# Optimization experiments

Hardware: AMD Instinct MI355X
Metric: run time of the kernel (lower is better)

The kernel has to match this reference:

```python
import jax, jax.numpy as jnp
import numpy as np

K = 3        # neighborhood kernel per spatial dim
DIL = 1      # dilation per spatial dim
NH = 8       # num heads
C = 64       # embed dims
EPS = 1e-5   # InstanceNorm eps


def _interp_axis(x, axis, out_len):
    # 1D linear interpolation with align_corners=True semantics
    in_len = x.shape[axis]
    pos = jnp.arange(out_len, dtype=jnp.float32) * ((in_len - 1) / (out_len - 1))
    i0 = jnp.clip(jnp.floor(pos).astype(jnp.int32), 0, in_len - 2)
    w = pos - i0.astype(jnp.float32)
    shape = [1] * x.ndim
    shape[axis] = out_len
    w = w.reshape(shape)
    return jnp.take(x, i0, axis=axis) * (1.0 - w) + jnp.take(x, i0 + 1, axis=axis) * w


def _upsample2_trilinear(x):
    # separable trilinear upsample x2 over the three spatial axes (2,3,4)
    for ax in (2, 3, 4):
        x = _interp_axis(x, ax, 2 * x.shape[ax])
    return x


def _instance_norm(t):
    # InstanceNorm3d, affine=False: normalize per (B,C) over spatial dims
    m = jnp.mean(t, axis=(2, 3, 4), keepdims=True)
    v = jnp.var(t, axis=(2, 3, 4), keepdims=True)
    return (t - m) * jax.lax.rsqrt(v + EPS)


def _nbr_idx(L, k, d):
    # NATTEN-style clamped neighborhood: window shifts to stay in-bounds at edges
    i = np.arange(L)
    start = np.clip(i - d * (k // 2), 0, L - d * (k - 1) - 1)
    idx = start[:, None] + np.arange(k)[None, :] * d          # (L,k) absolute nbr index
    rel = (idx - i[:, None]) // d + (k - 1)                   # (L,k) rel-pos-bias index in [0,2k-2]
    return jnp.asarray(idx), jnp.asarray(rel)


def _nca3d(qs, kv, Wq, bq, Wk, bk, Wv, bv, Wo, bo, rpb):
    # qs, kv: (B,H,W,Z,C) channels-last; q from skip, k/v from upsampled x
    B, H, W, Z, Cc = qs.shape
    dh = Cc // NH
    scale = dh ** -0.5
    q = (qs @ Wq + bq).reshape(B, H, W, Z, NH, dh) * scale
    k = (kv @ Wk + bk).reshape(B, H, W, Z, NH, dh)
    v = (kv @ Wv + bv).reshape(B, H, W, Z, NH, dh)

    ih, rh = _nbr_idx(H, K, DIL)
    iw, rw = _nbr_idx(W, K, DIL)
    iz, rz = _nbr_idx(Z, K, DIL)

    def gather_nbrs(t):
        t = jnp.take(t, ih, axis=1)   # (B,H,k,W,Z,nh,dh)
        t = jnp.take(t, iw, axis=3)   # (B,H,k,W,k,Z,nh,dh)
        t = jnp.take(t, iz, axis=5)   # (B,H,k,W,k,Z,k,nh,dh)
        t = jnp.transpose(t, (0, 1, 3, 5, 7, 2, 4, 6, 8))
        return t.reshape(B, H, W, Z, NH, K * K * K, dh)

    kg = gather_nbrs(k)
    vg = gather_nbrs(v)

    logits = jnp.einsum('bxyzhd,bxyzhmd->bxyzhm', q, kg)  # (B,H,W,Z,nh,27)

    # relative position bias: rpb (nh, 2k-1, 2k-1, 2k-1) gathered per query position
    bias = rpb[:, rh]                    # (nh,H,k,2k-1,2k-1)
    bias = jnp.take(bias, rw, axis=3)    # (nh,H,k,W,k,2k-1)
    bias = jnp.take(bias, rz, axis=5)    # (nh,H,k,W,k,Z,k)
    bias = jnp.transpose(bias, (1, 3, 5, 0, 2, 4, 6)).reshape(H, W, Z, NH, K * K * K)

    attn = jax.nn.softmax(logits + bias, axis=-1)
    o = jnp.einsum('bxyzhm,bxyzhmd->bxyzhd', attn, vg).reshape(B, H, W, Z, Cc)
    o = o @ Wo + bo
    return jnp.transpose(o, (0, 4, 1, 2, 3))  # back to (B,C,H,W,Z)


def setup_inputs() -> dict:
    key = jax.random.key(0)
    ks = jax.random.split(key, 8)
    s = 1.0 / np.sqrt(C)
    inp = {
        'x': jax.random.normal(ks[0], (1, C, 32, 32, 8), dtype=jnp.float32),
        'skip': jax.random.normal(ks[1], (1, C, 64, 64, 16), dtype=jnp.float32),
        'Wq': jax.random.normal(ks[2], (C, C), dtype=jnp.float32) * s,
        'bq': jnp.zeros((C,), dtype=jnp.float32),
        'Wk': jax.random.normal(ks[3], (C, C), dtype=jnp.float32) * s,
        'bk': jnp.zeros((C,), dtype=jnp.float32),
        'Wv': jax.random.normal(ks[4], (C, C), dtype=jnp.float32) * s,
        'bv': jnp.zeros((C,), dtype=jnp.float32),
        'Wo': jax.random.normal(ks[5], (C, C), dtype=jnp.float32) * s,
        'bo': jnp.zeros((C,), dtype=jnp.float32),
        'rpb': jax.random.normal(ks[6], (NH, 2 * K - 1, 2 * K - 1, 2 * K - 1), dtype=jnp.float32) * 0.02,
    }
    return inp


def reference(x, skip, Wq, bq, Wk, bk, Wv, bv, Wo, bo, rpb):
    xu = _instance_norm(_upsample2_trilinear(x))   # (B,C,2H,2W,2Z) == skip shape
    sk = _instance_norm(skip)
    qs = jnp.transpose(sk, (0, 2, 3, 4, 1))        # queries from skip
    kv = jnp.transpose(xu, (0, 2, 3, 4, 1))        # keys/values from upsampled x
    return _nca3d(qs, kv, Wq, bq, Wk, bk, Wv, bv, Wo, bo, rpb)
```

## Files before the change

### kernel.cpp

```cpp
#include <hip/hip_runtime.h>
#include <hip/hip_bf16.h>

typedef __hip_bfloat16 bf16;
typedef __attribute__((ext_vector_type(8))) short short8;

static constexpr int NPOS = 65536;

__device__ __forceinline__ float bs2f(short s) {
  union { float f; unsigned u; } cv;
  cv.u = ((unsigned)(unsigned short)s) << 16;
  return cv.f;
}
__device__ __forceinline__ short f2bs(float f) {
  bf16 b = __float2bfloat16(f);
  short r;
  __builtin_memcpy(&r, &b, 2);
  return r;
}

__global__ __launch_bounds__(256) void k_partial(const float* __restrict__ x,
                                                 const float* __restrict__ skip,
                                                 bf16* __restrict__ xu,
                                                 float* __restrict__ partials) {
  __shared__ float s1[256];
  __shared__ float s2[256];
  int b = blockIdx.x, tid = threadIdx.x;
  float sum = 0.f, sq = 0.f;
  if (b < 1024) {
    int c = b >> 4;
    int h = (b & 15) * 4 + (tid >> 6);
    int w = tid & 63;
    float fh = (float)h * (31.0f / 63.0f);
    int ih = (int)fh; if (ih > 30) ih = 30;
    float wh = fh - (float)ih;
    float fw = (float)w * (31.0f / 63.0f);
    int iw = (int)fw; if (iw > 30) iw = 30;
    float ww = fw - (float)iw;
    const float* base = x + c * 8192 + ih * 256 + iw * 8;
    float4 A0 = *(const float4*)(base);
    float4 A1 = *(const float4*)(base + 4);
    float4 B0 = *(const float4*)(base + 8);
    float4 B1 = *(const float4*)(base + 12);
    float4 C0 = *(const float4*)(base + 256);
    float4 C1 = *(const float4*)(base + 260);
    float4 D0 = *(const float4*)(base + 264);
    float4 D1 = *(const float4*)(base + 268);
    float ra[8] = {A0.x, A0.y, A0.z, A0.w, A1.x, A1.y, A1.z, A1.w};
    float rb[8] = {B0.x, B0.y, B0.z, B0.w, B1.x, B1.y, B1.z, B1.w};
    float rc[8] = {C0.x, C0.y, C0.z, C0.w, C1.x, C1.y, C1.z, C1.w};
    float rd[8] = {D0.x, D0.y, D0.z, D0.w, D1.x, D1.y, D1.z, D1.w};
    short8 o0, o1;
#pragma unroll
    for (int z = 0; z < 16; z++) {
      float fz = (float)z * (7.0f / 15.0f);
      int iz = (int)fz; if (iz > 6) iz = 6;
      float wz = fz - (float)iz;
      float va = ra[iz] * (1.f - wz) + ra[iz + 1] * wz;
      float vb = rb[iz] * (1.f - wz) + rb[iz + 1] * wz;
      float vc = rc[iz] * (1.f - wz) + rc[iz + 1] * wz;
      float vd = rd[iz] * (1.f - wz) + rd[iz + 1] * wz;
      float v0 = va * (1.f - ww) + vb * ww;
      float v1 = vc * (1.f - ww) + vd * ww;
      float v = v0 * (1.f - wh) + v1 * wh;
      sum += v; sq += v * v;
      if (z < 8) o0[z] = f2bs(v); else o1[z - 8] = f2bs(v);
    }
    bf16* xo = xu + (size_t)c * NPOS + h * 1024 + w * 16;
    *(short8*)xo = o0;
    *(short8*)(xo + 8) = o1;
  } else {
    int bb = b - 1024;
    const float4* p =
        (const float4*)(skip + (size_t)(bb >> 4) * NPOS + (bb & 15) * 4096);
    for (int i = tid; i < 1024; i += 256) {
      float4 v = p[i];
      sum += v.x + v.y + v.z + v.w;
      sq += v.x * v.x + v.y * v.y + v.z * v.z + v.w * v.w;
    }
  }
  s1[tid] = sum; s2[tid] = sq;
  __syncthreads();
  for (int s = 128; s > 0; s >>= 1) {
    if (tid < s) { s1[tid] += s1[tid + s]; s2[tid] += s2[tid + s]; }
    __syncthreads();
  }
  if (tid == 0) { partials[2 * b] = s1[0]; partials[2 * b + 1] = s2[0]; }
}

__global__ __launch_bounds__(128) void k_finalize(const float* __restrict__ partials,
                                                  float* __restrict__ stats) {
  int t = threadIdx.x;
  int base = (t < 64) ? t * 16 : 1024 + (t - 64) * 16;
  float sum = 0.f, sq = 0.f;
#pragma unroll
  for (int j = 0; j < 16; j++) {
    sum += partials[2 * (base + j)];
    sq  += partials[2 * (base + j) + 1];
  }
  float m = sum * (1.0f / NPOS);
  float var = sq * (1.0f / NPOS) - m * m;
  int off = (t < 64) ? 0 : 128;
  int c = t & 63;
  stats[off + c] = m;
  stats[off + 64 + c] = rsqrtf(var + 1e-5f);
}

__global__ __launch_bounds__(256) void k_proj_kvq(
    const bf16* __restrict__ xu, const float* __restrict__ skip,
    const float* __restrict__ stats,
    const float* __restrict__ Wk, const float* __restrict__ bk,
    const float* __restrict__ Wv, const float* __restrict__ bv,
    const float* __restrict__ Wq, const float* __restrict__ bq,
    bf16* __restrict__ kbuf, bf16* __restrict__ vbuf, bf16* __restrict__ qbuf) {
  __shared__ float xt[4096];
  int tid = threadIdx.x;
  int p0 = blockIdx.x * 64;
  for (int ii = tid; ii < 512; ii += 256) {
    int c = ii >> 3, t0 = (ii & 7) * 8;
    short8 v8 = *(const short8*)(xu + (size_t)c * NPOS + p0 + t0);
    float m = stats[c], r = stats[64 + c];
#pragma unroll
    for (int u = 0; u < 8; u++) xt[c * 64 + t0 + u] = (bs2f(v8[u]) - m) * r;
  }
  __syncthreads();
  int t = tid & 63;
  int j0 = __builtin_amdgcn_readfirstlane((tid >> 6) * 16);
  size_t p = (size_t)(p0 + t);
  float a[16];
  short8 s0, s1v;

#pragma unroll
  for (int u = 0; u < 16; u++) a[u] = bk[j0 + u];
  for (int c = 0; c < 64; c++) {
    float xv = xt[c * 64 + t];
    const float* wr = Wk + c * 64 + j0;
#pragma unroll
    for (int u = 0; u < 16; u++) a[u] += xv * wr[u];
  }
#pragma unroll
  for (int u = 0; u < 8; u++) { s0[u] = f2bs(a[u]); s1v[u] = f2bs(a[8 + u]); }
  *(short8*)(kbuf + p * 64 + j0) = s0;
  *(short8*)(kbuf + p * 64 + j0 + 8) = s1v;

#pragma unroll
  for (int u = 0; u < 16; u++) a[u] = bv[j0 + u];
  for (int c = 0; c < 64; c++) {
    float xv = xt[c * 64 + t];
    const float* wr = Wv + c * 64 + j0;
#pragma unroll
    for (int u = 0; u < 16; u++) a[u] += xv * wr[u];
  }
#pragma unroll
  for (int u = 0; u < 8; u++) { s0[u] = f2bs(a[u]); s1v[u] = f2bs(a[8 + u]); }
  *(short8*)(vbuf + p * 64 + j0) = s0;
  *(short8*)(vbuf + p * 64 + j0 + 8) = s1v;

  __syncthreads();
  for (int ii = tid; ii < 1024; ii += 256) {
    int c = ii >> 4, t0 = (ii & 15) * 4;
    float4 v = *(const float4*)(skip + (size_t)c * NPOS + p0 + t0);
    float m = stats[128 + c], r = stats[192 + c];
    xt[c * 64 + t0]     = (v.x - m) * r;
    xt[c * 64 + t0 + 1] = (v.y - m) * r;
    xt[c * 64 + t0 + 2] = (v.z - m) * r;
    xt[c * 64 + t0 + 3] = (v.w - m) * r;
  }
  __syncthreads();

  const float scale = 0.35355339059327373f;
#pragma unroll
  for (int u = 0; u < 16; u++) a[u] = bq[j0 + u];
  for (int c = 0; c < 64; c++) {
    float xv = xt[c * 64 + t];
    const float* wr = Wq + c * 64 + j0;
#pragma unroll
    for (int u = 0; u < 16; u++) a[u] += xv * wr[u];
  }
#pragma unroll
  for (int u = 0; u < 8; u++) {
    s0[u] = f2bs(a[u] * scale); s1v[u] = f2bs(a[8 + u] * scale);
  }
  *(short8*)(qbuf + p * 64 + j0) = s0;
  *(short8*)(qbuf + p * 64 + j0 + 8) = s1v;
}

__global__ __launch_bounds__(512, 2) void k_attn(
    const bf16* __restrict__ qbuf, const bf16* __restrict__ kbuf,
    const bf16* __restrict__ vbuf,
    const float* __restrict__ Wo, const float* __restrict__ bo,
    const float* __restrict__ rpb, float* __restrict__ out) {
  __shared__ float rp[1000];
  __shared__ float oT[64 * 65];
  int tid = threadIdx.x;
  int b = blockIdx.x;
  int sb = ((b & 7) << 7) + (b >> 3);
  int p0 = sb * 64;
  for (int i = tid; i < 1000; i += 512) rp[i] = rpb[i];
  __syncthreads();

  int head = tid & 7, pp = tid >> 3;
  int p = p0 + pp;
  int h = p >> 10, w = (p >> 4) & 63, z = p & 15;

  short8 q8 = *(const short8*)(qbuf + (size_t)p * 64 + head * 8);
  float q[8];
#pragma unroll
  for (int d = 0; d < 8; d++) q[d] = bs2f(q8[d]);

  int sh = h - 1; if (sh < 0) sh = 0; if (sh > 61) sh = 61;
  int sw = w - 1; if (sw < 0) sw = 0; if (sw > 61) sw = 61;
  int sz = z - 1; if (sz < 0) sz = 0; if (sz > 13) sz = 13;

  const bf16* kb = kbuf + (size_t)(sh * 1024 + sw * 16 + sz) * 64 + head * 8;
  const bf16* vb = vbuf + (size_t)(sh * 1024 + sw * 16 + sz) * 64 + head * 8;
  int rbase = ((sh - h + 2) * 5 + (sw - w + 2)) * 5 + (sz - z + 2) + head * 125;

  float s[27];
#pragma unroll
  for (int j = 0; j < 27; j++) {
    int kh = j / 9, kw = (j % 9) / 3, kz = j % 3;
    int coff = (kh * 1024 + kw * 16 + kz) * 64;
    short8 k8 = *(const short8*)(kb + coff);
    float sv = q[0] * bs2f(k8[0]) + q[1] * bs2f(k8[1]) +
               q[2] * bs2f(k8[2]) + q[3] * bs2f(k8[3]) +
               q[4] * bs2f(k8[4]) + q[5] * bs2f(k8[5]) +
               q[6] * bs2f(k8[6]) + q[7] * bs2f(k8[7]);
    s[j] = sv + rp[rbase + (kh * 5 + kw) * 5 + kz];
  }
  float M = s[26];
#pragma unroll
  for (int j = 0; j < 13; j++) M = fmaxf(M, fmaxf(s[2 * j], s[2 * j + 1]));

  float lrun = 0.f;
  float oa[8];
#pragma unroll
  for (int d = 0; d < 8; d++) oa[d] = 0.f;
#pragma unroll
  for (int j = 0; j < 27; j++) {
    int kh = j / 9, kw = (j % 9) / 3, kz = j % 3;
    int coff = (kh * 1024 + kw * 16 + kz) * 64;
    short8 v8 = *(const short8*)(vb + coff);
    float pw = __expf(s[j] - M);
    lrun += pw;
#pragma unroll
    for (int d = 0; d < 8; d++) oa[d] += pw * bs2f(v8[d]);
  }
  float inv = 1.0f / lrun;
#pragma unroll
  for (int d = 0; d < 8; d++) oT[pp * 65 + head * 8 + d] = oa[d] * inv;
  __syncthreads();

  int wid = __builtin_amdgcn_readfirstlane(tid >> 6);
  int l = tid & 63;
  float acc[8];
#pragma unroll
  for (int u = 0; u < 8; u++) acc[u] = bo[wid * 8 + u];
  for (int j = 0; j < 64; j++) {
    float ov = oT[l * 65 + j];
    const float* wr = Wo + j * 64 + wid * 8;
#pragma unroll
    for (int u = 0; u < 8; u++) acc[u] += ov * wr[u];
  }
#pragma unroll
  for (int u = 0; u < 8; u++)
    out[(size_t)(wid * 8 + u) * NPOS + p0 + l] = acc[u];
}

extern "C" void kernel_launch(void* const* d_in, const int* in_sizes, int n_in,
                              void* d_out, int out_size, void* d_ws, size_t ws_size,
                              hipStream_t stream) {
  const float* x    = (const float*)d_in[0];
  const float* skip = (const float*)d_in[1];
  const float* Wq   = (const float*)d_in[2];
  const float* bq   = (const float*)d_in[3];
  const float* Wk   = (const float*)d_in[4];
  const float* bk   = (const float*)d_in[5];
  const float* Wv   = (const float*)d_in[6];
  const float* bv   = (const float*)d_in[7];
  const float* Wo   = (const float*)d_in[8];
  const float* bo   = (const float*)d_in[9];
  const float* rpb  = (const float*)d_in[10];

  bf16* xu        = (bf16*)d_ws;
  bf16* kbuf      = (bf16*)((char*)d_ws + ((size_t)8 << 20));
  bf16* vbuf      = (bf16*)((char*)d_ws + ((size_t)16 << 20));
  bf16* qbuf      = (bf16*)((char*)d_ws + ((size_t)24 << 20));
  float* stats    = (float*)((char*)d_ws + ((size_t)32 << 20));
  float* partials = stats + 256;
  float* out = (float*)d_out;

  hipLaunchKernelGGL(k_partial, dim3(2048), dim3(256), 0, stream, x, skip, xu,
                     partials);
  hipLaunchKernelGGL(k_finalize, dim3(1), dim3(128), 0, stream, partials, stats);
  hipLaunchKernelGGL(k_proj_kvq, dim3(1024), dim3(256), 0, stream, xu, skip,
                     stats, Wk, bk, Wv, bv, Wq, bq, kbuf, vbuf, qbuf);
  hipLaunchKernelGGL(k_attn, dim3(1024), dim3(512), 0, stream, qbuf, kbuf, vbuf,
                     Wo, bo, rpb, out);
}
```

Measured before the change: 159.7 us.

## Use bf16 MFMA for QKV projections and fold stats finalize into projection kernel

Replaces the scalar FP32 FMA loops of the K/V/Q projections with bf16 MFMA 16x16x32 instructions. Activations and weights are staged in padded LDS tiles, and outputs are written to LDS and then stored with coalesced stores. The separate single-block finalize kernel is removed: each projection block recomputes the per-channel mean and rstd from the partial sums, which saves a launch and a serial tiny kernel. In exchange, inputs and weights are rounded to bf16 before the matmul, which lowers precision, and every block redundantly reads the partials and converts the weights.

```diff
diff --git a/kernel.cpp b/kernel.cpp
--- a/kernel.cpp
+++ b/kernel.cpp
@@ -3,6 +3,7 @@
 
 typedef __hip_bfloat16 bf16;
 typedef __attribute__((ext_vector_type(8))) short short8;
+typedef __attribute__((ext_vector_type(4))) float f32x4;
 
 static constexpr int NPOS = 65536;
 
@@ -87,101 +88,161 @@
   if (tid == 0) { partials[2 * b] = s1[0]; partials[2 * b + 1] = s2[0]; }
 }
 
-__global__ __launch_bounds__(128) void k_finalize(const float* __restrict__ partials,
-                                                  float* __restrict__ stats) {
-  int t = threadIdx.x;
-  int base = (t < 64) ? t * 16 : 1024 + (t - 64) * 16;
-  float sum = 0.f, sq = 0.f;
-#pragma unroll
-  for (int j = 0; j < 16; j++) {
-    sum += partials[2 * (base + j)];
-    sq  += partials[2 * (base + j) + 1];
-  }
-  float m = sum * (1.0f / NPOS);
-  float var = sq * (1.0f / NPOS) - m * m;
-  int off = (t < 64) ? 0 : 128;
-  int c = t & 63;
-  stats[off + c] = m;
-  stats[off + 64 + c] = rsqrtf(var + 1e-5f);
-}
-
-__global__ __launch_bounds__(256) void k_proj_kvq(
+__global__ __launch_bounds__(256) void k_proj_mfma(
     const bf16* __restrict__ xu, const float* __restrict__ skip,
-    const float* __restrict__ stats,
+    const float* __restrict__ partials,
     const float* __restrict__ Wk, const float* __restrict__ bk,
     const float* __restrict__ Wv, const float* __restrict__ bv,
     const float* __restrict__ Wq, const float* __restrict__ bq,
     bf16* __restrict__ kbuf, bf16* __restrict__ vbuf, bf16* __restrict__ qbuf) {
-  __shared__ float xt[4096];
+  __shared__ float stl[256];
+  __shared__ short xa[64 * 72];
+  __shared__ short wb[64 * 72];
+  __shared__ short ob[64 * 72];
   int tid = threadIdx.x;
   int p0 = blockIdx.x * 64;
+
+  if (tid < 128) {
+    int isk = tid >> 6, c = tid & 63;
+    int base = isk ? (1024 + c * 16) : (c * 16);
+    float sum = 0.f, sq = 0.f;
+#pragma unroll
+    for (int j = 0; j < 16; j++) {
+      sum += partials[2 * (base + j)];
+      sq  += partials[2 * (base + j) + 1];
+    }
+    float m = sum * (1.0f / NPOS);
+    float var = sq * (1.0f / NPOS) - m * m;
+    stl[isk * 128 + c] = m;
+    stl[isk * 128 + 64 + c] = rsqrtf(var + 1e-5f);
+  }
+  __syncthreads();
+
   for (int ii = tid; ii < 512; ii += 256) {
     int c = ii >> 3, t0 = (ii & 7) * 8;
     short8 v8 = *(const short8*)(xu + (size_t)c * NPOS + p0 + t0);
-    float m = stats[c], r = stats[64 + c];
-#pragma unroll
-    for (int u = 0; u < 8; u++) xt[c * 64 + t0 + u] = (bs2f(v8[u]) - m) * r;
-  }
-  __syncthreads();
-  int t = tid & 63;
-  int j0 = __builtin_amdgcn_readfirstlane((tid >> 6) * 16);
-  size_t p = (size_t)(p0 + t);
-  float a[16];
-  short8 s0, s1v;
-
-#pragma unroll
-  for (int u = 0; u < 16; u++) a[u] = bk[j0 + u];
-  for (int c = 0; c < 64; c++) {
-    float xv = xt[c * 64 + t];
-    const float* wr = Wk + c * 64 + j0;
-#pragma unroll
-    for (int u = 0; u < 16; u++) a[u] += xv * wr[u];
-  }
-#pragma unroll
-  for (int u = 0; u < 8; u++) { s0[u] = f2bs(a[u]); s1v[u] = f2bs(a[8 + u]); }
-  *(short8*)(kbuf + p * 64 + j0) = s0;
-  *(short8*)(kbuf + p * 64 + j0 + 8) = s1v;
-
-#pragma unroll
-  for (int u = 0; u < 16; u++) a[u] = bv[j0 + u];
-  for (int c = 0; c < 64; c++) {
-    float xv = xt[c * 64 + t];
-    const float* wr = Wv + c * 64 + j0;
-#pragma unroll
-    for (int u = 0; u < 16; u++) a[u] += xv * wr[u];
-  }
-#pragma unroll
-  for (int u = 0; u < 8; u++) { s0[u] = f2bs(a[u]); s1v[u] = f2bs(a[8 + u]); }
-  *(short8*)(vbuf + p * 64 + j0) = s0;
-  *(short8*)(vbuf + p * 64 + j0 + 8) = s1v;
-
-  __syncthreads();
+    float m = stl[c], r = stl[64 + c];
+#pragma unroll
+    for (int u = 0; u < 8; u++) xa[(t0 + u) * 72 + c] = f2bs((bs2f(v8[u]) - m) * r);
+  }
+  {
+    int c = tid >> 2, j0 = (tid & 3) * 16;
+    const float4* wr = (const float4*)(Wk + c * 64 + j0);
+    float4 w0 = wr[0], w1 = wr[1], w2 = wr[2], w3 = wr[3];
+    float wv[16] = {w0.x,w0.y,w0.z,w0.w, w1.x,w1.y,w1.z,w1.w,
+                    w2.x,w2.y,w2.z,w2.w, w3.x,w3.y,w3.z,w3.w};
+#pragma unroll
+    for (int u = 0; u < 16; u++) wb[(j0 + u) * 72 + c] = f2bs(wv[u]);
+  }
+  __syncthreads();
+
+  int wv_ = tid >> 6, lane = tid & 63, quad = lane >> 4, l15 = lane & 15;
+  const short* arow = &xa[(wv_ * 16 + l15) * 72 + quad * 8];
+  int orow0 = (wv_ * 16 + quad * 4);
+
+  {
+    short8 a0 = *(const short8*)(arow);
+    short8 a1 = *(const short8*)(arow + 32);
+#pragma unroll
+    for (int nt = 0; nt < 4; nt++) {
+      const short* brow = &wb[(nt * 16 + l15) * 72 + quad * 8];
+      short8 b0 = *(const short8*)(brow);
+      short8 b1 = *(const short8*)(brow + 32);
+      f32x4 acc = {0.f, 0.f, 0.f, 0.f};
+      acc = __builtin_amdgcn_mfma_f32_16x16x32_bf16(a0, b0, acc, 0, 0, 0);
+      acc = __builtin_amdgcn_mfma_f32_16x16x32_bf16(a1, b1, acc, 0, 0, 0);
+      float bval = bk[nt * 16 + l15];
+#pragma unroll
+      for (int r = 0; r < 4; r++)
+        ob[(orow0 + r) * 72 + nt * 16 + l15] = f2bs(acc[r] + bval);
+    }
+  }
+  __syncthreads();
+  {
+    int row = tid >> 2, col0 = (tid & 3) * 16;
+    short8 o0 = *(const short8*)(&ob[row * 72 + col0]);
+    short8 o1 = *(const short8*)(&ob[row * 72 + col0 + 8]);
+    *(short8*)(kbuf + (size_t)(p0 + row) * 64 + col0) = o0;
+    *(short8*)(kbuf + (size_t)(p0 + row) * 64 + col0 + 8) = o1;
+    int c = tid >> 2, j0 = (tid & 3) * 16;
+    const float4* wr = (const float4*)(Wv + c * 64 + j0);
+    float4 w0 = wr[0], w1 = wr[1], w2 = wr[2], w3 = wr[3];
+    float wvv[16] = {w0.x,w0.y,w0.z,w0.w, w1.x,w1.y,w1.z,w1.w,
+                     w2.x,w2.y,w2.z,w2.w, w3.x,w3.y,w3.z,w3.w};
+#pragma unroll
+    for (int u = 0; u < 16; u++) wb[(j0 + u) * 72 + c] = f2bs(wvv[u]);
+  }
+  __syncthreads();
+  {
+    short8 a0 = *(const short8*)(arow);
+    short8 a1 = *(const short8*)(arow + 32);
+#pragma unroll
+    for (int nt = 0; nt < 4; nt++) {
+      const short* brow = &wb[(nt * 16 + l15) * 72 + quad * 8];
+      short8 b0 = *(const short8*)(brow);
+      short8 b1 = *(const short8*)(brow + 32);
+      f32x4 acc = {0.f, 0.f, 0.f, 0.f};
+      acc = __builtin_amdgcn_mfma_f32_16x16x32_bf16(a0, b0, acc, 0, 0, 0);
+      acc = __builtin_amdgcn_mfma_f32_16x16x32_bf16(a1, b1, acc, 0, 0, 0);
+      float bval = bv[nt * 16 + l15];
+#pragma unroll
+      for (int r = 0; r < 4; r++)
+        ob[(orow0 + r) * 72 + nt * 16 + l15] = f2bs(acc[r] + bval);
+    }
+  }
+  __syncthreads();
+  {
+    int row = tid >> 2, col0 = (tid & 3) * 16;
+    short8 o0 = *(const short8*)(&ob[row * 72 + col0]);
+    short8 o1 = *(const short8*)(&ob[row * 72 + col0 + 8]);
+    *(short8*)(vbuf + (size_t)(p0 + row) * 64 + col0) = o0;
+    *(short8*)(vbuf + (size_t)(p0 + row) * 64 + col0 + 8) = o1;
+  }
   for (int ii = tid; ii < 1024; ii += 256) {
     int c = ii >> 4, t0 = (ii & 15) * 4;
     float4 v = *(const float4*)(skip + (size_t)c * NPOS + p0 + t0);
-    float m = stats[128 + c], r = stats[192 + c];
-    xt[c * 64 + t0]     = (v.x - m) * r;
-    xt[c * 64 + t0 + 1] = (v.y - m) * r;
-    xt[c * 64 + t0 + 2] = (v.z - m) * r;
-    xt[c * 64 + t0 + 3] = (v.w - m) * r;
-  }
-  __syncthreads();
-
-  const float scale = 0.35355339059327373f;
-#pragma unroll
-  for (int u = 0; u < 16; u++) a[u] = bq[j0 + u];
-  for (int c = 0; c < 64; c++) {
-    float xv = xt[c * 64 + t];
-    const float* wr = Wq + c * 64 + j0;
-#pragma unroll
-    for (int u = 0; u < 16; u++) a[u] += xv * wr[u];
-  }
-#pragma unroll
-  for (int u = 0; u < 8; u++) {
-    s0[u] = f2bs(a[u] * scale); s1v[u] = f2bs(a[8 + u] * scale);
-  }
-  *(short8*)(qbuf + p * 64 + j0) = s0;
-  *(short8*)(qbuf + p * 64 + j0 + 8) = s1v;
+    float m = stl[128 + c], r = stl[192 + c];
+    xa[(t0 + 0) * 72 + c] = f2bs((v.x - m) * r);
+    xa[(t0 + 1) * 72 + c] = f2bs((v.y - m) * r);
+    xa[(t0 + 2) * 72 + c] = f2bs((v.z - m) * r);
+    xa[(t0 + 3) * 72 + c] = f2bs((v.w - m) * r);
+  }
+  {
+    int c = tid >> 2, j0 = (tid & 3) * 16;
+    const float4* wr = (const float4*)(Wq + c * 64 + j0);
+    float4 w0 = wr[0], w1 = wr[1], w2 = wr[2], w3 = wr[3];
+    float wq_[16] = {w0.x,w0.y,w0.z,w0.w, w1.x,w1.y,w1.z,w1.w,
+                     w2.x,w2.y,w2.z,w2.w, w3.x,w3.y,w3.z,w3.w};
+#pragma unroll
+    for (int u = 0; u < 16; u++) wb[(j0 + u) * 72 + c] = f2bs(wq_[u]);
+  }
+  __syncthreads();
+  {
+    const float scale = 0.35355339059327373f;
+    short8 a0 = *(const short8*)(arow);
+    short8 a1 = *(const short8*)(arow + 32);
+#pragma unroll
+    for (int nt = 0; nt < 4; nt++) {
+      const short* brow = &wb[(nt * 16 + l15) * 72 + quad * 8];
+      short8 b0 = *(const short8*)(brow);
+      short8 b1 = *(const short8*)(brow + 32);
+      f32x4 acc = {0.f, 0.f, 0.f, 0.f};
+      acc = __builtin_amdgcn_mfma_f32_16x16x32_bf16(a0, b0, acc, 0, 0, 0);
+      acc = __builtin_amdgcn_mfma_f32_16x16x32_bf16(a1, b1, acc, 0, 0, 0);
+      float bval = bq[nt * 16 + l15];
+#pragma unroll
+      for (int r = 0; r < 4; r++)
+        ob[(orow0 + r) * 72 + nt * 16 + l15] = f2bs((acc[r] + bval) * scale);
+    }
+  }
+  __syncthreads();
+  {
+    int row = tid >> 2, col0 = (tid & 3) * 16;
+    short8 o0 = *(const short8*)(&ob[row * 72 + col0]);
+    short8 o1 = *(const short8*)(&ob[row * 72 + col0 + 8]);
+    *(short8*)(qbuf + (size_t)(p0 + row) * 64 + col0) = o0;
+    *(short8*)(qbuf + (size_t)(p0 + row) * 64 + col0 + 8) = o1;
+  }
 }
 
 __global__ __launch_bounds__(512, 2) void k_attn(
@@ -285,15 +346,13 @@
   bf16* kbuf      = (bf16*)((char*)d_ws + ((size_t)8 << 20));
   bf16* vbuf      = (bf16*)((char*)d_ws + ((size_t)16 << 20));
   bf16* qbuf      = (bf16*)((char*)d_ws + ((size_t)24 << 20));
-  float* stats    = (float*)((char*)d_ws + ((size_t)32 << 20));
-  float* partials = stats + 256;
+  float* partials = (float*)((char*)d_ws + ((size_t)32 << 20));
   float* out = (float*)d_out;
 
   hipLaunchKernelGGL(k_partial, dim3(2048), dim3(256), 0, stream, x, skip, xu,
                      partials);
-  hipLaunchKernelGGL(k_finalize, dim3(1), dim3(128), 0, stream, partials, stats);
-  hipLaunchKernelGGL(k_proj_kvq, dim3(1024), dim3(256), 0, stream, xu, skip,
-                     stats, Wk, bk, Wv, bv, Wq, bq, kbuf, vbuf, qbuf);
+  hipLaunchKernelGGL(k_proj_mfma, dim3(1024), dim3(256), 0, stream, xu, skip,
+                     partials, Wk, bk, Wv, bv, Wq, bq, kbuf, vbuf, qbuf);
   hipLaunchKernelGGL(k_attn, dim3(1024), dim3(512), 0, stream, qbuf, kbuf, vbuf,
                      Wo, bo, rpb, out);
 }
```

Result: faster. 147.5 us (-7.6%).
